# Optimization experiments

Measured on AMD Instinct MI355X. Metric: run time of the kernel, lower is better.

Reference implementation:

```python
import jax, jax.numpy as jnp
import numpy as np

B, N, K = 8, 2048, 64
RADII = (0.1, 0.3, 0.7)
TU = 256   # t_net_units
U = 512    # mmtsc_units
BLK = [(512, 512), (512, 256), (256, 170)]  # pce_depth=3, filters U//(i+1)
EPS = 1e-3  # keras BatchNormalization epsilon
BN_SCALE = np.float32(1.0 / np.sqrt(1.0 + EPS))  # inference BN: mean=0, var=1


def bn(x, g, b):
    return x * (g * BN_SCALE) + b


def setup_inputs():
    key = jax.random.key(0)
    ks = jax.random.split(key, 32)
    r = lambda i, sh, s=0.1: jax.random.normal(ks[i], sh, dtype=jnp.float32) * s
    inp = {
        "points": jax.random.normal(ks[0], (B, N, 3), dtype=jnp.float32),
        "noise": jax.random.uniform(ks[1], (B, N, N), dtype=jnp.float32),
        "tw": r(2, (3, TU)), "tb": r(3, (TU,)),
        "tg1": 1.0 + r(4, (TU,)), "tbt1": r(5, (TU,)),
        "td1w": r(6, (TU, TU)), "td1b": r(7, (TU,)),
        "tg2": 1.0 + r(8, (TU,)), "tbt2": r(9, (TU,)),
        "td2w": r(10, (TU, 9), 0.01), "td2b": jnp.ones((9,), jnp.float32),
        "c1w": r(11, (3 * K * 3, U)), "c1b": r(12, (U,)),
        "g1": 1.0 + r(13, (U,)), "be1": r(14, (U,)),
        "rw": r(15, (U, U)), "rb": r(16, (U,)),
    }
    for i, (ci, co) in enumerate(BLK):
        j = 17 + 4 * i
        inp[f"b{i+1}w"] = r(j, (ci, co))
        inp[f"b{i+1}b"] = r(j + 1, (co,))
        inp[f"b{i+1}g"] = 1.0 + r(j + 2, (co,))
        inp[f"b{i+1}be"] = r(j + 3, (co,))
    return inp


def reference(points, noise, tw, tb, tg1, tbt1, td1w, td1b, tg2, tbt2, td2w, td2b,
              c1w, c1b, g1, be1, rw, rb,
              b1w, b1b, b1g, b1be, b2w, b2b, b2g, b2be, b3w, b3b, b3g, b3be):
    relu = jax.nn.relu
    # ---- T-Net (dropout inactive at inference) ----
    x = relu(bn(points @ tw + tb, tg1, tbt1))       # [B,N,TU] (1x1 conv)
    x = jnp.max(x, axis=1)                          # GlobalMaxPooling1D -> [B,TU]
    x = relu(bn(x @ td1w + td1b, tg2, tbt2))        # [B,TU]
    T = (x @ td2w + td2b).reshape(-1, 3, 3)         # [B,3,3]
    pts = points @ T                                # [B,N,3]
    # ---- pairwise distances + multi-scale ball query ----
    diff = pts[:, :, None, :] - pts[:, None, :, :]  # [B,N,N,3]
    d = jax.lax.stop_gradient(jnp.sqrt(jnp.sum(diff * diff, axis=-1)))  # [B,N,N]
    bidx = jnp.arange(B)[:, None, None]
    groups = []
    for rad in RADII:
        score = jnp.where(d <= rad, noise, 0.0)     # mask * uniform
        idx = jnp.argsort(-score, axis=-1)[:, :, :K]  # descending, top-K  [B,N,K]
        groups.append(pts[bidx, idx])               # gather -> [B,N,K,3]
    feats = jnp.concatenate(groups, axis=-1).reshape(B, N, 3 * K * 3)  # [B,N,576]
    # ---- MLP stack (1x1 convs) ----
    f = relu(bn(feats @ c1w + c1b, g1, be1))        # [B,N,U]
    f = f + (f @ rw + rb)                           # residual
    for w, b_, g, be in ((b1w, b1b, b1g, b1be), (b2w, b2b, b2g, b2be), (b3w, b3b, b3g, b3be)):
        f = relu(bn(f @ w + b_, g, be))
    return jnp.max(f, axis=1)                       # [B,170]
```

## Files before the change

### kernel.cpp

```cpp
#include <hip/hip_runtime.h>
#include <hip/hip_bf16.h>


#define BN_SCALE 0.99950037468777f

typedef short short8 __attribute__((ext_vector_type(8)));
typedef float floatx4 __attribute__((ext_vector_type(4)));

#define OFF_FEATS 0
#define OFF_W     18874368
#define OFF_C1WT  (OFF_W)
#define OFF_RWT   (OFF_C1WT + 589824)
#define OFF_B1WT  (OFF_RWT + 524288)
#define OFF_B2WT  (OFF_B1WT + 524288)
#define OFF_B3WT  (OFF_B2WT + 262144)
#define OFF_PTS   (OFF_B3WT + 131072)
#define OFF_PART  (OFF_PTS + 196608)

__device__ inline short f2bf(float x) {
    __hip_bfloat16 h = __float2bfloat16(x);
    return *reinterpret_cast<short*>(&h);
}
__device__ inline float bf2f(short s) {
    return __uint_as_float(((unsigned)(unsigned short)s) << 16);
}

__global__ __launch_bounds__(256)
void convw_t_k(const float* __restrict__ c1w, const float* __restrict__ rw,
               const float* __restrict__ b1w, const float* __restrict__ b2w,
               const float* __restrict__ b3w,
               short* __restrict__ c1wT, short* __restrict__ rwT,
               short* __restrict__ b1wT, short* __restrict__ b2wT,
               short* __restrict__ b3wT) {
    __shared__ float tile[64][65];
    int bid = blockIdx.x;
    const float* src; short* dst; int K, N, t;
    if (bid < 72)       { src = c1w; dst = c1wT; K = 576; N = 512; t = bid; }
    else if (bid < 136) { src = rw;  dst = rwT;  K = 512; N = 512; t = bid - 72; }
    else if (bid < 200) { src = b1w; dst = b1wT; K = 512; N = 512; t = bid - 136; }
    else if (bid < 232) { src = b2w; dst = b2wT; K = 512; N = 256; t = bid - 200; }
    else                { src = b3w; dst = b3wT; K = 256; N = 170; t = bid - 232; }
    int ktiles = K >> 6;
    int k0 = (t % ktiles) * 64, n0 = (t / ktiles) * 64;
    int tx = threadIdx.x & 63, ty = threadIdx.x >> 6;
#pragma unroll
    for (int p = 0; p < 16; p++) {
        int r = p * 4 + ty;
        int n = n0 + tx;
        tile[r][tx] = (n < N) ? src[(size_t)(k0 + r) * N + n] : 0.f;
    }
    __syncthreads();
#pragma unroll
    for (int p = 0; p < 16; p++) {
        int r = p * 4 + ty;
        dst[(size_t)(n0 + r) * K + k0 + tx] = f2bf(tile[tx][r]);
    }
}

__global__ __launch_bounds__(256)
void tnet1_k(const float* __restrict__ points, const float* __restrict__ tw,
             const float* __restrict__ tb, const float* __restrict__ tg1,
             const float* __restrict__ tbt1, float* __restrict__ part) {
    const int b = blockIdx.y;
    const int u = threadIdx.x;
    const float w0 = tw[u], w1 = tw[256 + u], w2 = tw[512 + u];
    const float bi = tb[u];
    const float gs = tg1[u] * BN_SCALE, bt = tbt1[u];
    const float* pb = points + ((size_t)b * 2048 + blockIdx.x * 256) * 3;
    float m = 0.f;
    for (int nn = 0; nn < 256; nn++) {
        float p0 = pb[nn * 3], p1 = pb[nn * 3 + 1], p2 = pb[nn * 3 + 2];
        float v = p0 * w0 + p1 * w1 + p2 * w2 + bi;
        v = fmaxf(v * gs + bt, 0.f);
        m = fmaxf(m, v);
    }
    part[((b * 8 + blockIdx.x) << 8) + u] = m;
}

__global__ __launch_bounds__(256)
void tnet2_k(const float* __restrict__ points, const float* __restrict__ part,
             const float* __restrict__ td1w, const float* __restrict__ td1b,
             const float* __restrict__ tg2, const float* __restrict__ tbt2,
             const float* __restrict__ td2w, const float* __restrict__ td2b,
             float* __restrict__ pts_out) {
    __shared__ float sx[256], sx2[256], sT[9];
    const int b = blockIdx.x;
    const int t = threadIdx.x;
    float m = 0.f;
#pragma unroll
    for (int c = 0; c < 8; c++) m = fmaxf(m, part[((b * 8 + c) << 8) + t]);
    sx[t] = m;
    __syncthreads();
    float s = td1b[t];
    for (int v = 0; v < 256; v++) s += sx[v] * td1w[v * 256 + t];
    sx2[t] = fmaxf(s * (tg2[t] * BN_SCALE) + tbt2[t], 0.f);
    __syncthreads();
    if (t < 9) {
        float s2 = td2b[t];
        for (int v = 0; v < 256; v++) s2 += sx2[v] * td2w[v * 9 + t];
        sT[t] = s2;
    }
    __syncthreads();
    for (int n = t; n < 2048; n += 256) {
        size_t idx = ((size_t)b * 2048 + n) * 3;
        float p0 = points[idx], p1 = points[idx + 1], p2 = points[idx + 2];
        pts_out[idx]     = p0 * sT[0] + p1 * sT[3] + p2 * sT[6];
        pts_out[idx + 1] = p0 * sT[1] + p1 * sT[4] + p2 * sT[7];
        pts_out[idx + 2] = p0 * sT[2] + p1 * sT[5] + p2 * sT[8];
    }
}

__device__ inline void ins_one(unsigned& llo, unsigned& lhi, unsigned vlo,
                               unsigned vhi, int upaddr, int lane) {
    unsigned long long lv = ((unsigned long long)lhi << 32) | llo;
    unsigned long long vv = ((unsigned long long)vhi << 32) | vlo;
    unsigned long long ltm = __ballot(lv < vv);
    if (ltm) {
        int p = __builtin_ctzll(ltm);
        unsigned uplo = (unsigned)__builtin_amdgcn_ds_bpermute(upaddr, (int)llo);
        unsigned uphi = (unsigned)__builtin_amdgcn_ds_bpermute(upaddr, (int)lhi);
        if (lane >= p) {
            llo = (lane == p) ? vlo : uplo;
            lhi = (lane == p) ? vhi : uphi;
        }
    }
}

__device__ inline void run_q(unsigned& llo, unsigned& lhi, unsigned long long& th,
                             unsigned klo, unsigned khi, unsigned long long qual,
                             int upaddr, int lane) {
    do {
        int src = __builtin_ctzll(qual);
        qual &= qual - 1;
        unsigned vlo = (unsigned)__builtin_amdgcn_readlane((int)klo, src);
        unsigned vhi = (unsigned)__builtin_amdgcn_readlane((int)khi, src);
        ins_one(llo, lhi, vlo, vhi, upaddr, lane);
    } while (qual);
    th = ((unsigned long long)(unsigned)__builtin_amdgcn_readlane((int)lhi, 63) << 32)
         | (unsigned)__builtin_amdgcn_readlane((int)llo, 63);
}

__device__ inline void init_radius(bool in, unsigned nb, unsigned klo, int lane,
                                   int upaddr, unsigned& llo, unsigned& lhi,
                                   unsigned long long& th) {
    unsigned long long inm = __ballot(in);
    int S = 64 - __builtin_popcountll(inm);
    int mbI = __builtin_amdgcn_mbcnt_hi((unsigned)(inm >> 32),
              __builtin_amdgcn_mbcnt_lo((unsigned)inm, 0));
    int mbS = lane - mbI;
    int dst = in ? (S + mbI) : mbS;
    llo = (unsigned)__builtin_amdgcn_ds_permute(dst << 2, in ? 0 : (int)klo);
    lhi = 0;
    if (inm) {
        do {
            int src = __builtin_ctzll(inm);
            inm &= inm - 1;
            unsigned vlo = (unsigned)__builtin_amdgcn_readlane((int)klo, src);
            unsigned vhi = (unsigned)__builtin_amdgcn_readlane((int)nb, src);
            ins_one(llo, lhi, vlo, vhi, upaddr, lane);
        } while (inm);
    }
    th = ((unsigned long long)(unsigned)__builtin_amdgcn_readlane((int)lhi, 63) << 32)
         | (unsigned)__builtin_amdgcn_readlane((int)llo, 63);
}

__global__ __launch_bounds__(1024)
void topk_feats_k(const float* __restrict__ pts, const float* __restrict__ noise,
                  short* __restrict__ feats) {
    __shared__ float sxp[2048], syp[2048], szp[2048];
    const int b = blockIdx.y;
    const int tid = threadIdx.x;
    const int lane = tid & 63;
    const int wave = tid >> 6;
    const int n = blockIdx.x * 16 + wave;
    const float* nrow = noise + ((size_t)b * 2048 + n) * 2048;
    float ncur = nrow[lane];
    float nnxt = nrow[64 + lane];
    for (int i = tid; i < 2048; i += 1024) {
        size_t p = ((size_t)b * 2048 + i) * 3;
        sxp[i] = pts[p];
        syp[i] = pts[p + 1];
        szp[i] = pts[p + 2];
    }
    __syncthreads();
    const float qx = sxp[n], qy = syp[n], qz = szp[n];
    const int upaddr = (lane - 1) << 2;

    unsigned L0lo, L0hi, L1lo, L1hi, L2lo, L2hi;
    unsigned long long th0, th1, th2;
    {
        float dx = qx - sxp[lane], dy = qy - syp[lane], dz = qz - szp[lane];
        float d = sqrtf(dx * dx + dy * dy + dz * dz);
        unsigned nb = __float_as_uint(ncur);
        unsigned klo = 2047 - lane;
        init_radius(d <= 0.1f, nb, klo, lane, upaddr, L0lo, L0hi, th0);
        init_radius(d <= 0.3f, nb, klo, lane, upaddr, L1lo, L1hi, th1);
        init_radius(d <= 0.7f, nb, klo, lane, upaddr, L2lo, L2hi, th2);
    }
    for (int base = 64; base < 2048; base += 64) {
        float cur = nnxt;
        if (base + 64 < 2048) nnxt = nrow[base + 64 + lane];
        const int j = base + lane;
        float dx = qx - sxp[j], dy = qy - syp[j], dz = qz - szp[j];
        float d = sqrtf(dx * dx + dy * dy + dz * dz);
        unsigned nb = __float_as_uint(cur);
        unsigned klo = 2047 - j;
        unsigned k0hi = (d <= 0.1f) ? nb : 0u;
        unsigned k1hi = (d <= 0.3f) ? nb : 0u;
        unsigned k2hi = (d <= 0.7f) ? nb : 0u;
        unsigned long long key0 = ((unsigned long long)k0hi << 32) | klo;
        unsigned long long key1 = ((unsigned long long)k1hi << 32) | klo;
        unsigned long long key2 = ((unsigned long long)k2hi << 32) | klo;
        unsigned long long q0 = __ballot(key0 > th0);
        unsigned long long q1 = __ballot(key1 > th1);
        unsigned long long q2 = __ballot(key2 > th2);
        if (q0) run_q(L0lo, L0hi, th0, klo, k0hi, q0, upaddr, lane);
        if (q1) run_q(L1lo, L1hi, th1, klo, k1hi, q1, upaddr, lane);
        if (q2) run_q(L2lo, L2hi, th2, klo, k2hi, q2, upaddr, lane);
    }
    size_t basef = ((size_t)b * 2048 + n) * 576 + (size_t)lane * 9;
    int j0 = 2047 - (int)(L0lo & 0x7FFu);
    int j1 = 2047 - (int)(L1lo & 0x7FFu);
    int j2 = 2047 - (int)(L2lo & 0x7FFu);
    feats[basef + 0] = f2bf(sxp[j0]);
    feats[basef + 1] = f2bf(syp[j0]);
    feats[basef + 2] = f2bf(szp[j0]);
    feats[basef + 3] = f2bf(sxp[j1]);
    feats[basef + 4] = f2bf(syp[j1]);
    feats[basef + 5] = f2bf(szp[j1]);
    feats[basef + 6] = f2bf(sxp[j2]);
    feats[basef + 7] = f2bf(syp[j2]);
    feats[basef + 8] = f2bf(szp[j2]);
}


__device__ inline int act_addr(int r, int c) {
    return r * 512 + ((((c >> 3) ^ (r & 7)) << 3) | (c & 7));
}

template <int KST, int JT>
__device__ inline void mm_lds(const short* __restrict__ act,
                              const short* __restrict__ BT, int K, int colbase,
                              int lr, int lq, floatx4 (&acc)[4][JT]) {
#pragma unroll 4
    for (int ks = 0; ks < KST; ks++) {
        short8 af[4], bf[JT];
        int g = ks * 4 + lq;
#pragma unroll
        for (int i = 0; i < 4; i++) {
            int r = i * 16 + lr;
            af[i] = *(const short8*)(act + r * 512 + ((g ^ (lr & 7)) << 3));
        }
#pragma unroll
        for (int j = 0; j < JT; j++)
            bf[j] = *(const short8*)(BT + (size_t)(colbase + j * 16 + lr) * K +
                                     ks * 32 + lq * 8);
#pragma unroll
        for (int i = 0; i < 4; i++)
#pragma unroll
            for (int j = 0; j < JT; j++)
                acc[i][j] = __builtin_amdgcn_mfma_f32_16x16x32_bf16(af[i], bf[j],
                                                                    acc[i][j], 0, 0, 0);
    }
}

template <int JT, bool RELU, bool RESID>
__device__ inline void epi_store(short* __restrict__ act, floatx4 (&acc)[4][JT],
                                 int colbase, int lr, int lq,
                                 const float* __restrict__ bias,
                                 const float* __restrict__ gamma,
                                 const float* __restrict__ beta) {
    short st[4][JT][4];
#pragma unroll
    for (int j = 0; j < JT; j++) {
        int c = colbase + j * 16 + lr;
        float bi = bias[c];
        float gs = RELU ? gamma[c] * BN_SCALE : 0.f;
        float bt = RELU ? beta[c] : 0.f;
#pragma unroll
        for (int i = 0; i < 4; i++)
#pragma unroll
            for (int reg = 0; reg < 4; reg++) {
                int r = i * 16 + lq * 4 + reg;
                float v = acc[i][j][reg] + bi;
                if (RESID) v += bf2f(act[act_addr(r, c)]);
                if (RELU) v = fmaxf(v * gs + bt, 0.f);
                st[i][j][reg] = f2bf(v);
            }
    }
    __syncthreads();
#pragma unroll
    for (int j = 0; j < JT; j++) {
        int c = colbase + j * 16 + lr;
#pragma unroll
        for (int i = 0; i < 4; i++)
#pragma unroll
            for (int reg = 0; reg < 4; reg++) {
                int r = i * 16 + lq * 4 + reg;
                act[act_addr(r, c)] = st[i][j][reg];
            }
    }
    __syncthreads();
}

__global__ __launch_bounds__(512)
void chain_k(const short* __restrict__ feats,
             const short* __restrict__ c1wT, const short* __restrict__ rwT,
             const short* __restrict__ b1wT, const short* __restrict__ b2wT,
             const short* __restrict__ b3wT,
             const float* __restrict__ c1b, const float* __restrict__ g1,
             const float* __restrict__ be1, const float* __restrict__ rb,
             const float* __restrict__ b1b, const float* __restrict__ b1g,
             const float* __restrict__ b1be,
             const float* __restrict__ b2b, const float* __restrict__ b2g,
             const float* __restrict__ b2be,
             const float* __restrict__ b3b, const float* __restrict__ b3g,
             const float* __restrict__ b3be,
             float* __restrict__ out) {
    __shared__ short act[64 * 512];
    const int tid = threadIdx.x;
    const int lane = tid & 63, wq = tid >> 6;
    const int lr = lane & 15, lq = lane >> 4;
    const long m0 = (long)blockIdx.x * 64;

    {
        floatx4 acc[4][4] = {};
        const short* Ab = feats + (m0 + lr) * 576 + lq * 8;
        const short* Bb = c1wT + (size_t)(wq * 64 + lr) * 576 + lq * 8;
#pragma unroll 4
        for (int ks = 0; ks < 18; ks++) {
            short8 af[4], bf[4];
#pragma unroll
            for (int i = 0; i < 4; i++)
                af[i] = *(const short8*)(Ab + (size_t)i * 16 * 576 + ks * 32);
#pragma unroll
            for (int j = 0; j < 4; j++)
                bf[j] = *(const short8*)(Bb + (size_t)j * 16 * 576 + ks * 32);
#pragma unroll
            for (int i = 0; i < 4; i++)
#pragma unroll
                for (int j = 0; j < 4; j++)
                    acc[i][j] = __builtin_amdgcn_mfma_f32_16x16x32_bf16(
                        af[i], bf[j], acc[i][j], 0, 0, 0);
        }
        epi_store<4, true, false>(act, acc, wq * 64, lr, lq, c1b, g1, be1);
    }
    {
        floatx4 acc[4][4] = {};
        mm_lds<16, 4>(act, rwT, 512, wq * 64, lr, lq, acc);
        epi_store<4, false, true>(act, acc, wq * 64, lr, lq, rb, nullptr, nullptr);
    }
    {
        floatx4 acc[4][4] = {};
        mm_lds<16, 4>(act, b1wT, 512, wq * 64, lr, lq, acc);
        epi_store<4, true, false>(act, acc, wq * 64, lr, lq, b1b, b1g, b1be);
    }
    {
        floatx4 acc[4][2] = {};
        mm_lds<16, 2>(act, b2wT, 512, wq * 32, lr, lq, acc);
        epi_store<2, true, false>(act, acc, wq * 32, lr, lq, b2b, b2g, b2be);
    }
    {
        floatx4 acc[4][2] = {};
        mm_lds<8, 2>(act, b3wT, 256, wq * 32, lr, lq, acc);
        const int bb = blockIdx.x >> 5;
#pragma unroll
        for (int j = 0; j < 2; j++) {
            int c = wq * 32 + j * 16 + lr;
            bool valid = (c < 170);
            float bi = valid ? b3b[c] : 0.f;
            float gs = valid ? b3g[c] * BN_SCALE : 0.f;
            float bt = valid ? b3be[c] : 0.f;
            float cm = 0.f;
#pragma unroll
            for (int i = 0; i < 4; i++)
#pragma unroll
                for (int reg = 0; reg < 4; reg++) {
                    float v = fmaxf((acc[i][j][reg] + bi) * gs + bt, 0.f);
                    cm = fmaxf(cm, v);
                }
            cm = fmaxf(cm, __shfl_xor(cm, 16));
            cm = fmaxf(cm, __shfl_xor(cm, 32));
            if (lq == 0 && valid)
                atomicMax((unsigned int*)&out[bb * 170 + c], __float_as_uint(cm));
        }
    }
}

extern "C" void kernel_launch(void* const* d_in, const int* in_sizes, int n_in,
                              void* d_out, int out_size, void* d_ws, size_t ws_size,
                              hipStream_t stream) {
    const float* points = (const float*)d_in[0];
    const float* noise  = (const float*)d_in[1];
    const float* tw   = (const float*)d_in[2];
    const float* tb   = (const float*)d_in[3];
    const float* tg1  = (const float*)d_in[4];
    const float* tbt1 = (const float*)d_in[5];
    const float* td1w = (const float*)d_in[6];
    const float* td1b = (const float*)d_in[7];
    const float* tg2  = (const float*)d_in[8];
    const float* tbt2 = (const float*)d_in[9];
    const float* td2w = (const float*)d_in[10];
    const float* td2b = (const float*)d_in[11];
    const float* c1w  = (const float*)d_in[12];
    const float* c1b  = (const float*)d_in[13];
    const float* g1   = (const float*)d_in[14];
    const float* be1  = (const float*)d_in[15];
    const float* rw   = (const float*)d_in[16];
    const float* rb   = (const float*)d_in[17];
    const float* b1w  = (const float*)d_in[18];
    const float* b1b  = (const float*)d_in[19];
    const float* b1g  = (const float*)d_in[20];
    const float* b1be = (const float*)d_in[21];
    const float* b2w  = (const float*)d_in[22];
    const float* b2b  = (const float*)d_in[23];
    const float* b2g  = (const float*)d_in[24];
    const float* b2be = (const float*)d_in[25];
    const float* b3w  = (const float*)d_in[26];
    const float* b3b  = (const float*)d_in[27];
    const float* b3g  = (const float*)d_in[28];
    const float* b3be = (const float*)d_in[29];

    char* ws = (char*)d_ws;
    short* feats = (short*)(ws + OFF_FEATS);
    short* c1wT  = (short*)(ws + OFF_C1WT);
    short* rwT   = (short*)(ws + OFF_RWT);
    short* b1wT  = (short*)(ws + OFF_B1WT);
    short* b2wT  = (short*)(ws + OFF_B2WT);
    short* b3wT  = (short*)(ws + OFF_B3WT);
    float* pts   = (float*)(ws + OFF_PTS);
    float* part  = (float*)(ws + OFF_PART);

    hipMemsetAsync(d_out, 0, (size_t)out_size * sizeof(float), stream);

    convw_t_k<<<248, 256, 0, stream>>>(c1w, rw, b1w, b2w, b3w,
                                       c1wT, rwT, b1wT, b2wT, b3wT);
    tnet1_k<<<dim3(8, 8), 256, 0, stream>>>(points, tw, tb, tg1, tbt1, part);
    tnet2_k<<<8, 256, 0, stream>>>(points, part, td1w, td1b, tg2, tbt2,
                                   td2w, td2b, pts);
    topk_feats_k<<<dim3(128, 8), 1024, 0, stream>>>(pts, noise, feats);
    chain_k<<<256, 512, 0, stream>>>(feats, c1wT, rwT, b1wT, b2wT, b3wT,
                                     c1b, g1, be1, rb, b1b, b1g, b1be,
                                     b2b, b2g, b2be, b3b, b3g, b3be,
                                     (float*)d_out);
}
```

Before: 463.1 us.

## Retile MLP chain to 32-row blocks with prefetch; parallelize T-Net kernels

The fused MLP chain kernel now handles 32 rows per block with 4 waves of 256 threads, each wave owning 128 columns, instead of 64 rows with 8 waves. Weight and activation fragments are double-buffered one k-step ahead, and the K loop is fully unrolled. This doubles the grid to 512 blocks and halves LDS per block, which should raise occupancy and hide global-load latency. The cost is more weight traffic per output row and higher register pressure. Separately, tnet1 stages its points in shared memory, and tnet2 splits its two small dense layers across 1024 threads with partial sums.

```diff
diff --git a/kernel.cpp b/kernel.cpp
--- a/kernel.cpp
+++ b/kernel.cpp
@@ -61,47 +61,75 @@
 void tnet1_k(const float* __restrict__ points, const float* __restrict__ tw,
              const float* __restrict__ tb, const float* __restrict__ tg1,
              const float* __restrict__ tbt1, float* __restrict__ part) {
+    __shared__ float spts[768];
     const int b = blockIdx.y;
     const int u = threadIdx.x;
+    const float* pb = points + ((size_t)b * 2048 + blockIdx.x * 256) * 3;
+    for (int i = u; i < 768; i += 256) spts[i] = pb[i];
     const float w0 = tw[u], w1 = tw[256 + u], w2 = tw[512 + u];
     const float bi = tb[u];
     const float gs = tg1[u] * BN_SCALE, bt = tbt1[u];
-    const float* pb = points + ((size_t)b * 2048 + blockIdx.x * 256) * 3;
+    __syncthreads();
     float m = 0.f;
     for (int nn = 0; nn < 256; nn++) {
-        float p0 = pb[nn * 3], p1 = pb[nn * 3 + 1], p2 = pb[nn * 3 + 2];
-        float v = p0 * w0 + p1 * w1 + p2 * w2 + bi;
+        float v = spts[nn * 3] * w0 + spts[nn * 3 + 1] * w1 +
+                  spts[nn * 3 + 2] * w2 + bi;
         v = fmaxf(v * gs + bt, 0.f);
         m = fmaxf(m, v);
     }
     part[((b * 8 + blockIdx.x) << 8) + u] = m;
 }
 
-__global__ __launch_bounds__(256)
+__global__ __launch_bounds__(1024)
 void tnet2_k(const float* __restrict__ points, const float* __restrict__ part,
              const float* __restrict__ td1w, const float* __restrict__ td1b,
              const float* __restrict__ tg2, const float* __restrict__ tbt2,
              const float* __restrict__ td2w, const float* __restrict__ td2b,
              float* __restrict__ pts_out) {
-    __shared__ float sx[256], sx2[256], sT[9];
+    __shared__ float sx[256], sp[4][256], sx2[256], sp2[9][32], sT[9];
     const int b = blockIdx.x;
-    const int t = threadIdx.x;
-    float m = 0.f;
-#pragma unroll
-    for (int c = 0; c < 8; c++) m = fmaxf(m, part[((b * 8 + c) << 8) + t]);
-    sx[t] = m;
-    __syncthreads();
-    float s = td1b[t];
-    for (int v = 0; v < 256; v++) s += sx[v] * td1w[v * 256 + t];
-    sx2[t] = fmaxf(s * (tg2[t] * BN_SCALE) + tbt2[t], 0.f);
-    __syncthreads();
-    if (t < 9) {
-        float s2 = td2b[t];
-        for (int v = 0; v < 256; v++) s2 += sx2[v] * td2w[v * 9 + t];
-        sT[t] = s2;
-    }
-    __syncthreads();
-    for (int n = t; n < 2048; n += 256) {
+    const int tid = threadIdx.x;
+    if (tid < 256) {
+        float m = 0.f;
+#pragma unroll
+        for (int c = 0; c < 8; c++) m = fmaxf(m, part[((b * 8 + c) << 8) + tid]);
+        sx[tid] = m;
+    }
+    __syncthreads();
+    {
+        int t = tid & 255, g = tid >> 8;
+        float s = 0.f;
+#pragma unroll 8
+        for (int i = 0; i < 64; i++) {
+            int v = g * 64 + i;
+            s += sx[v] * td1w[v * 256 + t];
+        }
+        sp[g][t] = s;
+    }
+    __syncthreads();
+    if (tid < 256) {
+        float s = td1b[tid] + sp[0][tid] + sp[1][tid] + sp[2][tid] + sp[3][tid];
+        sx2[tid] = fmaxf(s * (tg2[tid] * BN_SCALE) + tbt2[tid], 0.f);
+    }
+    __syncthreads();
+    if (tid < 288) {
+        int j = tid / 32, vg = tid & 31;
+        float s = 0.f;
+#pragma unroll
+        for (int i = 0; i < 8; i++) {
+            int v = vg * 8 + i;
+            s += sx2[v] * td2w[v * 9 + j];
+        }
+        sp2[j][vg] = s;
+    }
+    __syncthreads();
+    if (tid < 9) {
+        float s = td2b[tid];
+        for (int vg = 0; vg < 32; vg++) s += sp2[tid][vg];
+        sT[tid] = s;
+    }
+    __syncthreads();
+    for (int n = tid; n < 2048; n += 1024) {
         size_t idx = ((size_t)b * 2048 + n) * 3;
         float p0 = points[idx], p1 = points[idx + 1], p2 = points[idx + 2];
         pts_out[idx]     = p0 * sT[0] + p1 * sT[3] + p2 * sT[6];
@@ -238,39 +266,46 @@
     return r * 512 + ((((c >> 3) ^ (r & 7)) << 3) | (c & 7));
 }
 
-template <int KST, int JT>
+template <int K, int JT>
 __device__ inline void mm_lds(const short* __restrict__ act,
-                              const short* __restrict__ BT, int K, int colbase,
-                              int lr, int lq, floatx4 (&acc)[4][JT]) {
-#pragma unroll 4
+                              const short* __restrict__ BT, int colbase,
+                              int lr, int lq, floatx4 (&acc)[2][JT]) {
+    constexpr int KST = K / 32;
+    const short* Bb = BT + (size_t)(colbase + lr) * K + lq * 8;
+    short8 bf[JT], bfn[JT];
+#pragma unroll
+    for (int j = 0; j < JT; j++) bf[j] = *(const short8*)(Bb + j * 16 * K);
+#pragma unroll
     for (int ks = 0; ks < KST; ks++) {
-        short8 af[4], bf[JT];
+        if (ks + 1 < KST) {
+#pragma unroll
+            for (int j = 0; j < JT; j++)
+                bfn[j] = *(const short8*)(Bb + j * 16 * K + (ks + 1) * 32);
+        }
+        short8 af[2];
         int g = ks * 4 + lq;
 #pragma unroll
-        for (int i = 0; i < 4; i++) {
-            int r = i * 16 + lr;
-            af[i] = *(const short8*)(act + r * 512 + ((g ^ (lr & 7)) << 3));
-        }
-#pragma unroll
-        for (int j = 0; j < JT; j++)
-            bf[j] = *(const short8*)(BT + (size_t)(colbase + j * 16 + lr) * K +
-                                     ks * 32 + lq * 8);
-#pragma unroll
-        for (int i = 0; i < 4; i++)
+        for (int i = 0; i < 2; i++)
+            af[i] = *(const short8*)(act + (i * 16 + lr) * 512 +
+                                     ((g ^ (lr & 7)) << 3));
+#pragma unroll
+        for (int i = 0; i < 2; i++)
 #pragma unroll
             for (int j = 0; j < JT; j++)
                 acc[i][j] = __builtin_amdgcn_mfma_f32_16x16x32_bf16(af[i], bf[j],
                                                                     acc[i][j], 0, 0, 0);
+#pragma unroll
+        for (int j = 0; j < JT; j++) bf[j] = bfn[j];
     }
 }
 
 template <int JT, bool RELU, bool RESID>
-__device__ inline void epi_store(short* __restrict__ act, floatx4 (&acc)[4][JT],
+__device__ inline void epi_store(short* __restrict__ act, floatx4 (&acc)[2][JT],
                                  int colbase, int lr, int lq,
                                  const float* __restrict__ bias,
                                  const float* __restrict__ gamma,
                                  const float* __restrict__ beta) {
-    short st[4][JT][4];
+    short st[2][JT][4];
 #pragma unroll
     for (int j = 0; j < JT; j++) {
         int c = colbase + j * 16 + lr;
@@ -278,7 +313,7 @@
         float gs = RELU ? gamma[c] * BN_SCALE : 0.f;
         float bt = RELU ? beta[c] : 0.f;
 #pragma unroll
-        for (int i = 0; i < 4; i++)
+        for (int i = 0; i < 2; i++)
 #pragma unroll
             for (int reg = 0; reg < 4; reg++) {
                 int r = i * 16 + lq * 4 + reg;
@@ -293,7 +328,7 @@
     for (int j = 0; j < JT; j++) {
         int c = colbase + j * 16 + lr;
 #pragma unroll
-        for (int i = 0; i < 4; i++)
+        for (int i = 0; i < 2; i++)
 #pragma unroll
             for (int reg = 0; reg < 4; reg++) {
                 int r = i * 16 + lq * 4 + reg;
@@ -303,7 +338,7 @@
     __syncthreads();
 }
 
-__global__ __launch_bounds__(512)
+__global__ __launch_bounds__(256)
 void chain_k(const short* __restrict__ feats,
              const short* __restrict__ c1wT, const short* __restrict__ rwT,
              const short* __restrict__ b1wT, const short* __restrict__ b2wT,
@@ -317,63 +352,73 @@
              const float* __restrict__ b3b, const float* __restrict__ b3g,
              const float* __restrict__ b3be,
              float* __restrict__ out) {
-    __shared__ short act[64 * 512];
+    __shared__ short act[32 * 512];
     const int tid = threadIdx.x;
     const int lane = tid & 63, wq = tid >> 6;
     const int lr = lane & 15, lq = lane >> 4;
-    const long m0 = (long)blockIdx.x * 64;
-
-    {
-        floatx4 acc[4][4] = {};
+    const long m0 = (long)blockIdx.x * 32;
+
+    {
+        floatx4 acc[2][8] = {};
         const short* Ab = feats + (m0 + lr) * 576 + lq * 8;
-        const short* Bb = c1wT + (size_t)(wq * 64 + lr) * 576 + lq * 8;
-#pragma unroll 4
+        const short* Bb = c1wT + (size_t)(wq * 128 + lr) * 576 + lq * 8;
+        short8 bf[8], bfn[8], af[2], afn[2];
+#pragma unroll
+        for (int j = 0; j < 8; j++) bf[j] = *(const short8*)(Bb + j * 16 * 576);
+#pragma unroll
+        for (int i = 0; i < 2; i++) af[i] = *(const short8*)(Ab + i * 16 * 576);
+#pragma unroll
         for (int ks = 0; ks < 18; ks++) {
-            short8 af[4], bf[4];
-#pragma unroll
-            for (int i = 0; i < 4; i++)
-                af[i] = *(const short8*)(Ab + (size_t)i * 16 * 576 + ks * 32);
-#pragma unroll
-            for (int j = 0; j < 4; j++)
-                bf[j] = *(const short8*)(Bb + (size_t)j * 16 * 576 + ks * 32);
-#pragma unroll
-            for (int i = 0; i < 4; i++)
-#pragma unroll
-                for (int j = 0; j < 4; j++)
+            if (ks + 1 < 18) {
+#pragma unroll
+                for (int j = 0; j < 8; j++)
+                    bfn[j] = *(const short8*)(Bb + j * 16 * 576 + (ks + 1) * 32);
+#pragma unroll
+                for (int i = 0; i < 2; i++)
+                    afn[i] = *(const short8*)(Ab + i * 16 * 576 + (ks + 1) * 32);
+            }
+#pragma unroll
+            for (int i = 0; i < 2; i++)
+#pragma unroll
+                for (int j = 0; j < 8; j++)
                     acc[i][j] = __builtin_amdgcn_mfma_f32_16x16x32_bf16(
                         af[i], bf[j], acc[i][j], 0, 0, 0);
-        }
-        epi_store<4, true, false>(act, acc, wq * 64, lr, lq, c1b, g1, be1);
-    }
-    {
-        floatx4 acc[4][4] = {};
-        mm_lds<16, 4>(act, rwT, 512, wq * 64, lr, lq, acc);
-        epi_store<4, false, true>(act, acc, wq * 64, lr, lq, rb, nullptr, nullptr);
-    }
-    {
-        floatx4 acc[4][4] = {};
-        mm_lds<16, 4>(act, b1wT, 512, wq * 64, lr, lq, acc);
-        epi_store<4, true, false>(act, acc, wq * 64, lr, lq, b1b, b1g, b1be);
-    }
-    {
-        floatx4 acc[4][2] = {};
-        mm_lds<16, 2>(act, b2wT, 512, wq * 32, lr, lq, acc);
-        epi_store<2, true, false>(act, acc, wq * 32, lr, lq, b2b, b2g, b2be);
-    }
-    {
-        floatx4 acc[4][2] = {};
-        mm_lds<8, 2>(act, b3wT, 256, wq * 32, lr, lq, acc);
-        const int bb = blockIdx.x >> 5;
-#pragma unroll
-        for (int j = 0; j < 2; j++) {
-            int c = wq * 32 + j * 16 + lr;
+#pragma unroll
+            for (int j = 0; j < 8; j++) bf[j] = bfn[j];
+#pragma unroll
+            for (int i = 0; i < 2; i++) af[i] = afn[i];
+        }
+        epi_store<8, true, false>(act, acc, wq * 128, lr, lq, c1b, g1, be1);
+    }
+    {
+        floatx4 acc[2][8] = {};
+        mm_lds<512, 8>(act, rwT, wq * 128, lr, lq, acc);
+        epi_store<8, false, true>(act, acc, wq * 128, lr, lq, rb, nullptr, nullptr);
+    }
+    {
+        floatx4 acc[2][8] = {};
+        mm_lds<512, 8>(act, b1wT, wq * 128, lr, lq, acc);
+        epi_store<8, true, false>(act, acc, wq * 128, lr, lq, b1b, b1g, b1be);
+    }
+    {
+        floatx4 acc[2][4] = {};
+        mm_lds<512, 4>(act, b2wT, wq * 64, lr, lq, acc);
+        epi_store<4, true, false>(act, acc, wq * 64, lr, lq, b2b, b2g, b2be);
+    }
+    {
+        floatx4 acc[2][4] = {};
+        mm_lds<256, 4>(act, b3wT, wq * 64, lr, lq, acc);
+        const int bb = blockIdx.x >> 6;
+#pragma unroll
+        for (int j = 0; j < 4; j++) {
+            int c = wq * 64 + j * 16 + lr;
             bool valid = (c < 170);
             float bi = valid ? b3b[c] : 0.f;
             float gs = valid ? b3g[c] * BN_SCALE : 0.f;
             float bt = valid ? b3be[c] : 0.f;
             float cm = 0.f;
 #pragma unroll
-            for (int i = 0; i < 4; i++)
+            for (int i = 0; i < 2; i++)
 #pragma unroll
                 for (int reg = 0; reg < 4; reg++) {
                     float v = fmaxf((acc[i][j][reg] + bi) * gs + bt, 0.f);
@@ -436,10 +481,10 @@
     convw_t_k<<<248, 256, 0, stream>>>(c1w, rw, b1w, b2w, b3w,
                                        c1wT, rwT, b1wT, b2wT, b3wT);
     tnet1_k<<<dim3(8, 8), 256, 0, stream>>>(points, tw, tb, tg1, tbt1, part);
-    tnet2_k<<<8, 256, 0, stream>>>(points, part, td1w, td1b, tg2, tbt2,
-                                   td2w, td2b, pts);
+    tnet2_k<<<8, 1024, 0, stream>>>(points, part, td1w, td1b, tg2, tbt2,
+                                    td2w, td2b, pts);
     topk_feats_k<<<dim3(128, 8), 1024, 0, stream>>>(pts, noise, feats);
-    chain_k<<<256, 512, 0, stream>>>(feats, c1wT, rwT, b1wT, b2wT, b3wT,
+    chain_k<<<512, 256, 0, stream>>>(feats, c1wT, rwT, b1wT, b2wT, b3wT,
                                      c1b, g1, be1, rb, b1b, b1g, b1be,
                                      b2b, b2g, b2be, b3b, b3g, b3be,
                                      (float*)d_out);
```

Measured after the change: 484.3 us. +4.6%, slower.
